# Kernel tuning notes

Measured on AMD Instinct MI355X. Metric: run time of the kernel, lower is better.

Reference implementation:

```python
import jax, jax.numpy as jnp
import numpy as np

J = 24          # SMPL_NR_JOINTS
H = 24          # hidden_dim
D_IN = 3        # input_dim (xyz)
SMPL_PARENTS = [-1, 0, 0, 0, 1, 2, 3, 4, 5, 6, 7, 8, 9, 9, 9, 12, 13, 14, 16, 17, 18, 19, 20, 21]

def _build_A():
    # undirected kinematic tree + self loops, row-normalized (mean aggregation)
    M = np.zeros((J, J), np.float32)
    for child, parent in enumerate(SMPL_PARENTS):
        if parent >= 0:
            M[child, parent] = 1.0
            M[parent, child] = 1.0
    M += np.eye(J, dtype=np.float32)
    M /= M.sum(axis=1, keepdims=True)
    return jnp.asarray(M)

A_NORM = _build_A()  # [J, J]

def setup_inputs() -> dict:
    key = jax.random.key(0)
    ks = jax.random.split(key, 12)
    B, S, T = 2048, 24, 24
    g = lambda k, shape, s=0.1: jax.random.normal(k, shape, dtype=jnp.float32) * s
    return {
        "src": g(ks[0], (B, S, J, D_IN), 1.0),
        "tgt": g(ks[1], (B, T, J, D_IN), 1.0),
        "We": g(ks[2], (H, D_IN)), "be": jnp.zeros((H,), jnp.float32),
        # gate order: 0=i, 1=f, 2=c, 3=o
        "Wxl": g(ks[3], (4, H, H)), "bxl": jnp.zeros((4, H), jnp.float32),
        "Wxr": g(ks[4], (4, H, H)),
        "Whl": g(ks[5], (4, H, H)), "bhl": jnp.zeros((4, H), jnp.float32),
        "Whr": g(ks[6], (4, H, H)),
        "wg": g(ks[7], (3, H)),   # peephole weights for i, f, o
        "bg": jnp.zeros((4, H), jnp.float32),
        "Wd": g(ks[8], (D_IN * J, H * J)), "bd": jnp.zeros((D_IN * J,), jnp.float32),
    }

def _gconv(x, Wl, bl, Wr):
    # x: [B, J, D]; mean-aggregate over fixed 24-node graph, then l(agg) + r(x)
    agg = jnp.einsum('ij,bjd->bid', A_NORM, x)
    return agg @ Wl.T + bl + x @ Wr.T

def _cell(X, h, c, Wxl, bxl, Wxr, Whl, bhl, Whr, wg, bg):
    gx = lambda g: _gconv(X, Wxl[g], bxl[g], Wxr[g])
    gh = lambda g: _gconv(h, Whl[g], bhl[g], Whr[g])
    i = jax.nn.sigmoid(gx(0) + gh(0) + wg[0] * c + bg[0])
    f = jax.nn.sigmoid(gx(1) + gh(1) + wg[1] * c + bg[1])
    c_new = f * c + i * jnp.tanh(gx(2) + gh(2) + bg[2])
    o = jax.nn.sigmoid(gx(3) + gh(3) + wg[2] * c_new + bg[3])
    h_new = o * jnp.tanh(c_new)
    return o, h_new, c_new

def reference(src, tgt, We, be, Wxl, bxl, Wxr, Whl, bhl, Whr, wg, bg, Wd, bd):
    B, S = src.shape[0], src.shape[1]
    T = tgt.shape[1]
    params = (Wxl, bxl, Wxr, Whl, bhl, Whr, wg, bg)
    enc = lambda x: jax.nn.relu(x @ We.T + be)  # [B, J, H]

    # --- warm-up over last 24 src frames (deterministic: encode only first step) ---
    X0 = enc(src[:, S - 24])
    h = jnp.zeros((B, J, H), src.dtype)
    c = jnp.zeros((B, J, H), src.dtype)
    out, h, c = _cell(X0, h, c, *params)

    def warm_step(carry, _):
        o_, h_, c_ = carry
        o_, h_, c_ = _cell(o_, h_, c_, *params)
        return (o_, h_, c_), None
    (out, h, c), _ = jax.lax.scan(warm_step, (out, h, c), None, length=23)

    # --- decode T steps: first input is enc(tgt[:,0]), then feed previous out ---
    out0, h, c = _cell(enc(tgt[:, 0]), h, c, *params)

    def dec_step(carry, _):
        o_, h_, c_ = carry
        o2, h2, c2 = _cell(o_, h_, c_, *params)
        return (o2, h2, c2), o2
    _, rest = jax.lax.scan(dec_step, (out0, h, c), None, length=T - 1)  # [T-1, B, J, H]

    seq = jnp.concatenate([out0[None], rest], axis=0)            # [T, B, J, H]
    outs = seq.transpose(1, 0, 2, 3).reshape(B, T, J * H)        # [B, T, 576]
    return outs @ Wd.T + bd                                      # [B, T, 72]
```

## Files before the change

### kernel.cpp

```cpp
#include <hip/hip_runtime.h>


typedef short  s16x8 __attribute__((ext_vector_type(8)));
typedef float  f32x4 __attribute__((ext_vector_type(4)));
typedef _Float16 f16x8 __attribute__((ext_vector_type(8)));

#define TPB 192
#define NB 2
#define PQ_OFF 0
#define UO_OFF 19968
#define SMEM_SZ 26880

#define BAR() do { asm volatile("s_waitcnt lgkmcnt(0)" ::: "memory"); \
                   __builtin_amdgcn_s_barrier(); } while (0)

__device__ __forceinline__ unsigned short f2h(float f) {
    _Float16 h = (_Float16)f;
    return *(unsigned short*)&h;
}
__device__ __forceinline__ unsigned int pkrtz(float a, float b) {
    auto h = __builtin_amdgcn_cvt_pkrtz(a, b);
    return *(unsigned int*)&h;
}
__device__ __forceinline__ float frcp(float x) { return __builtin_amdgcn_rcpf(x); }
__device__ __forceinline__ float sigm(float x) {
    float t = __expf(-x);
    return frcp(1.0f + t);
}
__device__ __forceinline__ float tanh_(float x) {
    float xc = fmaxf(x, -30.f);
    float t = __expf(-2.f * xc);
    return (1.f - t) * frcp(1.f + t);
}

extern "C" __global__ void __launch_bounds__(TPB, 3)
gclstm_main(const float* __restrict__ src,
            const float* __restrict__ tgt,
            const float* __restrict__ We,
            const float* __restrict__ be,
            const float* __restrict__ Wxl,
            const float* __restrict__ bxl,
            const float* __restrict__ Wxr,
            const float* __restrict__ Whl,
            const float* __restrict__ bhl,
            const float* __restrict__ Whr,
            const float* __restrict__ wg,
            const float* __restrict__ bg,
            unsigned short* __restrict__ seqh)
{
    __shared__ __align__(16) char smem[SMEM_SZ];
    unsigned short* PQt  = (unsigned short*)(smem + PQ_OFF);
    unsigned short* UO   = (unsigned short*)(smem + UO_OFF);
    unsigned int*   UO32 = (unsigned int*)(smem + UO_OFF);

    const int tid = threadIdx.x;
    const int b0 = blockIdx.x * NB;
    const int lane = tid & 63, wid = tid >> 6;
    const int l15 = lane & 15, quad = lane >> 4;

    const int par[24] = {-1,0,0,0,1,2,3,4,5,6,7,8,9,9,9,12,13,14,16,17,18,19,20,21};

    f16x8 w1f[4][2];
#pragma unroll
    for (int cj = 0; cj < 4; ++cj) {
        int np = (wid * 4 + cj) * 16 + l15;
        int path = np >= 96 ? 1 : 0;
        int nn = np - path * 96;
        int g = nn / 24, d = nn - g * 24;
        const float* Wx = path ? Wxr : Wxl;
        const float* Wh = path ? Whr : Whl;
#pragma unroll
        for (int kt = 0; kt < 2; ++kt) {
            f16x8 f;
#pragma unroll
            for (int kk = 0; kk < 8; ++kk) {
                int k = kt * 32 + quad * 8 + kk;
                float v = 0.f;
                if (k < 48) {
                    int df = k >> 1;
                    v = (k & 1) ? Wh[g * 576 + d * 24 + df] : Wx[g * 576 + d * 24 + df];
                }
                f[kk] = (_Float16)v;
            }
            w1f[cj][kt] = f;
        }
    }

    f16x8 mf[3];
    {
        int i = wid * 16 + l15;
        int si = i / 24, ji = i - si * 24;
        int cnt = 1 + (par[ji] >= 0 ? 1 : 0);
#pragma unroll
        for (int ch = 0; ch < 24; ++ch) cnt += (par[ch] == ji) ? 1 : 0;
        float cntf = (float)cnt;
#pragma unroll
        for (int kt = 0; kt < 3; ++kt) {
            f16x8 f;
#pragma unroll
            for (int kk = 0; kk < 8; ++kk) {
                int jp = kt * 32 + quad * 8 + kk;
                int sj = jp / 48;
                int rem = jp - sj * 48;
                int pz = rem / 24;
                int j = rem - pz * 24;
                float v = 0.f;
                if (sj == si) {
                    if (pz == 0) v = (j == ji || par[j] == ji || par[ji] == j) ? 1.f : 0.f;
                    else         v = (j == ji) ? cntf : 0.f;
                }
                f[kk] = (_Float16)v;
            }
            mf[kt] = f;
        }
    }

    const int d1 = l15;
    const int d2 = 16 + (l15 & 7);
    const bool lo = l15 < 8;
    float bC1[4], bC2[4], wv1[3], wv2[3];
#pragma unroll
    for (int g = 0; g < 4; ++g) {
        bC1[g] = bxl[g * 24 + d1] + bhl[g * 24 + d1] + bg[g * 24 + d1];
        bC2[g] = bxl[g * 24 + d2] + bhl[g * 24 + d2] + bg[g * 24 + d2];
    }
#pragma unroll
    for (int p = 0; p < 3; ++p) { wv1[p] = wg[p * 24 + d1]; wv2[p] = wg[p * 24 + d2]; }

    int rowR[4];
    float iwR[4];
    unsigned int sb[4];
#pragma unroll
    for (int rr = 0; rr < 4; ++rr) {
        int row = wid * 16 + quad * 4 + rr;
        rowR[rr] = row;
        int j = row % 24;
        int cnt = 1 + (par[j] >= 0 ? 1 : 0);
#pragma unroll
        for (int ch = 0; ch < 24; ++ch) cnt += (par[ch] == j) ? 1 : 0;
        iwR[rr] = cnt == 2 ? 0.5f : cnt == 3 ? (1.f / 3.f) : cnt == 4 ? 0.25f : 0.2f;
        sb[rr] = (unsigned int)((b0 + row / 24) * 13824 + j * 24);
    }
    int row2v[2]; float iw2v[2]; unsigned int sb2v[2];
#pragma unroll
    for (int e = 0; e < 2; ++e) {
        int rsel = lo ? e : e + 2;
        row2v[e] = rowR[rsel]; iw2v[e] = iwR[rsel]; sb2v[e] = sb[rsel];
    }

    float c1[4] = {0.f, 0.f, 0.f, 0.f};
    float c2[2] = {0.f, 0.f};

#pragma unroll
    for (int t = 0; t < 3; ++t) {
        int task = tid + t * TPB;
        int row = task / 12, dp = task - row * 12;
        int b = b0 + row / 24, j = row % 24;
        const float* sp = src + (size_t)b * 1728 + j * 3;
        float s0 = sp[0], s1 = sp[1], s2 = sp[2];
        int d = 2 * dp;
        float x0 = be[d] + s0 * We[d * 3] + s1 * We[d * 3 + 1] + s2 * We[d * 3 + 2];
        float x1 = be[d + 1] + s0 * We[d * 3 + 3] + s1 * We[d * 3 + 4] + s2 * We[d * 3 + 5];
        x0 = fmaxf(x0, 0.f); x1 = fmaxf(x1, 0.f);
        uint2 wv; wv.x = pkrtz(x0, 0.f); wv.y = pkrtz(x1, 0.f);
        *(uint2*)(UO32 + row * 36 + 2 * dp) = wv;
    }
    {
        int row = tid >> 2, c = tid & 3;
        uint2 z; z.x = 0u; z.y = 0u;
        *(uint2*)(UO32 + row * 36 + 24 + 2 * c) = z;
    }
    __syncthreads();

    for (int s = 0; s < 48; ++s) {
        if (s == 24) {
#pragma unroll
            for (int t = 0; t < 3; ++t) {
                int task = tid + t * TPB;
                int row = task / 12, dp = task - row * 12;
                int b = b0 + row / 24, j = row % 24;
                const float* tp = tgt + (size_t)b * 1728 + j * 3;
                float s0 = tp[0], s1 = tp[1], s2 = tp[2];
                int d = 2 * dp;
                float x0 = be[d] + s0 * We[d * 3] + s1 * We[d * 3 + 1] + s2 * We[d * 3 + 2];
                float x1 = be[d + 1] + s0 * We[d * 3 + 3] + s1 * We[d * 3 + 4]
                         + s2 * We[d * 3 + 5];
                x0 = fmaxf(x0, 0.f); x1 = fmaxf(x1, 0.f);
                UO[row * 72 + 4 * dp] = f2h(x0);
                UO[row * 72 + 4 * dp + 2] = f2h(x1);
            }
            BAR();
        }

        f32x4 acc1[3][4];
#pragma unroll
        for (int rt = 0; rt < 3; ++rt)
#pragma unroll
            for (int cj = 0; cj < 4; ++cj) acc1[rt][cj] = (f32x4)0.f;
#pragma unroll
        for (int kt = 0; kt < 2; ++kt) {
            f16x8 a[3];
#pragma unroll
            for (int rt = 0; rt < 3; ++rt)
                a[rt] = *(const f16x8*)(UO + (rt * 16 + l15) * 72 + kt * 32 + quad * 8);
#pragma unroll
            for (int rt = 0; rt < 3; ++rt)
#pragma unroll
                for (int cj = 0; cj < 4; ++cj)
                    acc1[rt][cj] = __builtin_amdgcn_mfma_f32_16x16x32_f16(a[rt], w1f[cj][kt], acc1[rt][cj], 0, 0, 0);
        }
#pragma unroll
        for (int rt = 0; rt < 3; ++rt)
#pragma unroll
            for (int cj = 0; cj < 4; ++cj) {
                int np = (wid * 4 + cj) * 16 + l15;
                int path = np >= 96;
                int nn = np - (path ? 96 : 0);
                int jg = rt * 16 + quad * 4;
                int col = (path ? 24 : 0) + jg + (jg >= 24 ? 24 : 0);
                uint2 wv;
                wv.x = pkrtz(acc1[rt][cj][0], acc1[rt][cj][1]);
                wv.y = pkrtz(acc1[rt][cj][2], acc1[rt][cj][3]);
                *(uint2*)(PQt + nn * 104 + col) = wv;
            }
        BAR();

        f32x4 acc2[6];
#pragma unroll
        for (int nt = 0; nt < 6; ++nt) acc2[nt] = (f32x4)0.f;
#pragma unroll
        for (int kt = 0; kt < 3; ++kt) {
            if (kt == 2 && wid == 0) continue;
            if (kt == 0 && wid == 2) continue;
            f16x8 bf[6];
#pragma unroll
            for (int nt = 0; nt < 6; ++nt)
                bf[nt] = *(const f16x8*)(PQt + (nt * 16 + l15) * 104 + kt * 32 + quad * 8);
#pragma unroll
            for (int nt = 0; nt < 6; ++nt)
                acc2[nt] = __builtin_amdgcn_mfma_f32_16x16x32_f16(mf[kt], bf[nt], acc2[nt], 0, 0, 0);
        }

        const int so = (s - 24) * 576;

#pragma unroll
        for (int rr = 0; rr < 4; ++rr) {
            float pf_s = __shfl_xor(lo ? acc2[2][rr] : acc2[1][rr], 8);
            float po_s = __shfl_xor(lo ? acc2[5][rr] : acc2[4][rr], 8);
            float iw = iwR[rr];
            int row = rowR[rr];
            float c = c1[rr];
            float pi = fmaf(iw, acc2[0][rr], bC1[0]);
            float pf = fmaf(iw, pf_s, bC1[1]);
            float pc = fmaf(iw, acc2[3][rr], bC1[2]);
            float po = fmaf(iw, po_s, bC1[3]);
            float iv = sigm(fmaf(wv1[0], c, pi));
            float fv = sigm(fmaf(wv1[1], c, pf));
            float cn = fmaf(fv, c, iv * tanh_(pc));
            float ov = sigm(fmaf(wv1[2], cn, po));
            c1[rr] = cn;
            float hv = ov * tanh_(cn);
            unsigned int pk = pkrtz(ov, hv);
            UO32[row * 36 + d1] = pk;
            if (s >= 24) seqh[sb[rr] + (unsigned int)(so + d1)] = (unsigned short)pk;
        }
#pragma unroll
        for (int e = 0; e < 2; ++e) {
            float sA = __shfl_xor(lo ? acc2[1][e + 2] : acc2[2][e], 8);
            float sB = __shfl_xor(lo ? acc2[4][e + 2] : acc2[5][e], 8);
            float g0 = lo ? acc2[1][e] : sA;
            float g1 = lo ? sA : acc2[2][e + 2];
            float g2 = lo ? acc2[4][e] : sB;
            float g3 = lo ? sB : acc2[5][e + 2];
            float iw = iw2v[e];
            int row = row2v[e];
            float c = c2[e];
            float pi = fmaf(iw, g0, bC2[0]);
            float pf = fmaf(iw, g1, bC2[1]);
            float pc = fmaf(iw, g2, bC2[2]);
            float po = fmaf(iw, g3, bC2[3]);
            float iv = sigm(fmaf(wv2[0], c, pi));
            float fv = sigm(fmaf(wv2[1], c, pf));
            float cn = fmaf(fv, c, iv * tanh_(pc));
            float ov = sigm(fmaf(wv2[2], cn, po));
            c2[e] = cn;
            float hv = ov * tanh_(cn);
            unsigned int pk = pkrtz(ov, hv);
            UO32[row * 36 + d2] = pk;
            if (s >= 24) seqh[sb2v[e] + (unsigned int)(so + d2)] = (unsigned short)pk;
        }
        BAR();
    }
}

extern "C" __global__ void __launch_bounds__(256)
wd_conv(const float* __restrict__ Wd, unsigned short* __restrict__ WdH)
{
    int i = blockIdx.x * 256 + threadIdx.x;
    if (i < 46080) {
        int n = i / 576, k = i - n * 576;
        WdH[i] = (n < 72) ? f2h(Wd[n * 576 + k]) : (unsigned short)0;
    }
}

template <int PRECONV>
__global__ void __launch_bounds__(256, 6)
gclstm_proj(const unsigned short* __restrict__ seqh,
            const unsigned short* __restrict__ WdH,
            const float* __restrict__ Wd,
            const float* __restrict__ bd,
            float* __restrict__ out)
{
    __shared__ unsigned short SQ[32 * 104];
    __shared__ unsigned short WH[80 * 104];

    const int tid = threadIdx.x;
    const int R0 = blockIdx.x * 32;
    const int lane = tid & 63, wid = tid >> 6;
    const int l15 = lane & 15, quad = lane >> 4;
    const int rt = wid & 1;
    const int c0 = (wid < 2) ? 0 : 3;
    const int nct = (wid < 2) ? 3 : 2;

    f32x4 acc[3];
#pragma unroll
    for (int j = 0; j < 3; ++j) acc[j] = (f32x4)0.f;

    if (PRECONV) {
        s16x8 sreg[2], wreg[4];
        const int r0s = tid / 12, c0s = tid - r0s * 12;
        const int i1 = tid + 256;
        const int r1s = i1 / 12, c1s = i1 - r1s * 12;
        sreg[0] = *(const s16x8*)(seqh + (size_t)(R0 + r0s) * 576 + (size_t)(c0s * 8));
        if (tid < 128)
            sreg[1] = *(const s16x8*)(seqh + (size_t)(R0 + r1s) * 576 + (size_t)(c1s * 8));
#pragma unroll
        for (int j = 0; j < 4; ++j) {
            int i = tid + j * 256;
            if (i < 960) { int n = i / 12, c8 = i - n * 12;
                wreg[j] = *(const s16x8*)(WdH + (size_t)n * 576 + (size_t)(c8 * 8)); }
        }
        for (int kc = 0; kc < 576; kc += 96) {
            *(s16x8*)(&SQ[r0s * 104 + c0s * 8]) = sreg[0];
            if (tid < 128) *(s16x8*)(&SQ[r1s * 104 + c1s * 8]) = sreg[1];
#pragma unroll
            for (int j = 0; j < 4; ++j) {
                int i = tid + j * 256;
                if (i < 960) { int n = i / 12, c8 = i - n * 12;
                    *(s16x8*)(&WH[n * 104 + c8 * 8]) = wreg[j]; }
            }
            BAR();
            if (kc + 96 < 576) {
                sreg[0] = *(const s16x8*)(seqh + (size_t)(R0 + r0s) * 576 + (size_t)(kc + 96 + c0s * 8));
                if (tid < 128)
                    sreg[1] = *(const s16x8*)(seqh + (size_t)(R0 + r1s) * 576 + (size_t)(kc + 96 + c1s * 8));
#pragma unroll
                for (int j = 0; j < 4; ++j) {
                    int i = tid + j * 256;
                    if (i < 960) { int n = i / 12, c8 = i - n * 12;
                        wreg[j] = *(const s16x8*)(WdH + (size_t)n * 576 + (size_t)(kc + 96 + c8 * 8)); }
                }
            }
#pragma unroll
            for (int kt = 0; kt < 3; ++kt) {
                int koff = kt * 32 + quad * 8;
                f16x8 a = *(const f16x8*)(&SQ[(rt * 16 + l15) * 104 + koff]);
#pragma unroll
                for (int j = 0; j < 3; ++j) {
                    if (j < nct) {
                        f16x8 b = *(const f16x8*)(&WH[((c0 + j) * 16 + l15) * 104 + koff]);
                        acc[j] = __builtin_amdgcn_mfma_f32_16x16x32_f16(a, b, acc[j], 0, 0, 0);
                    }
                }
            }
            BAR();
        }
    } else {
        for (int kc = 0; kc < 576; kc += 96) {
            __syncthreads();
            for (int i = tid; i < 384; i += 256) {
                int r = i / 12, c8 = i - r * 12;
                *(s16x8*)(&SQ[r * 104 + c8 * 8]) =
                    *(const s16x8*)(seqh + (size_t)(R0 + r) * 576 + (size_t)(kc + c8 * 8));
            }
            for (int i = tid; i < 7680; i += 256) {
                int n = i / 96, kk = i - n * 96;
                float v = (n < 72) ? Wd[(size_t)n * 576 + (size_t)(kc + kk)] : 0.f;
                WH[n * 104 + kk] = f2h(v);
            }
            __syncthreads();
#pragma unroll
            for (int kt = 0; kt < 3; ++kt) {
                int koff = kt * 32 + quad * 8;
                f16x8 a = *(const f16x8*)(&SQ[(rt * 16 + l15) * 104 + koff]);
#pragma unroll
                for (int j = 0; j < 3; ++j) {
                    if (j < nct) {
                        f16x8 b = *(const f16x8*)(&WH[((c0 + j) * 16 + l15) * 104 + koff]);
                        acc[j] = __builtin_amdgcn_mfma_f32_16x16x32_f16(a, b, acc[j], 0, 0, 0);
                    }
                }
            }
        }
    }

#pragma unroll
    for (int j = 0; j < 3; ++j) {
        if (j < nct) {
            int n = (c0 + j) * 16 + l15;
            if (n < 72) {
                float bv = bd[n];
                int rbase = R0 + rt * 16 + quad * 4;
#pragma unroll
                for (int r = 0; r < 4; ++r)
                    out[(size_t)(rbase + r) * 72 + (size_t)n] = acc[j][r] + bv;
            }
        }
    }
}

extern "C" void kernel_launch(void* const* d_in, const int* in_sizes, int n_in,
                              void* d_out, int out_size, void* d_ws, size_t ws_size,
                              hipStream_t stream)
{
    const float* src = (const float*)d_in[0];
    const float* tgt = (const float*)d_in[1];
    const float* We  = (const float*)d_in[2];
    const float* be  = (const float*)d_in[3];
    const float* Wxl = (const float*)d_in[4];
    const float* bxl = (const float*)d_in[5];
    const float* Wxr = (const float*)d_in[6];
    const float* Whl = (const float*)d_in[7];
    const float* bhl = (const float*)d_in[8];
    const float* Whr = (const float*)d_in[9];
    const float* wg  = (const float*)d_in[10];
    const float* bg  = (const float*)d_in[11];
    const float* Wd  = (const float*)d_in[12];
    const float* bd  = (const float*)d_in[13];
    float* out = (float*)d_out;
    unsigned short* seqh = (unsigned short*)d_ws;

    const size_t seq_bytes = (size_t)2048 * 24 * 576 * 2;
    unsigned short* WdH = (unsigned short*)((char*)d_ws + seq_bytes);
    const bool preconv = ws_size >= seq_bytes + (size_t)80 * 576 * 2;

    if (preconv)
        wd_conv<<<dim3(180), dim3(256), 0, stream>>>(Wd, WdH);
    gclstm_main<<<dim3(1024), dim3(TPB), 0, stream>>>(
        src, tgt, We, be, Wxl, bxl, Wxr, Whl, bhl, Whr, wg, bg, seqh);
    if (preconv)
        gclstm_proj<1><<<dim3(1536), dim3(256), 0, stream>>>(seqh, WdH, Wd, bd, out);
    else
        gclstm_proj<0><<<dim3(1536), dim3(256), 0, stream>>>(seqh, nullptr, Wd, bd, out);
}
```

Measured before the change: 328.3 us.

## Replace LDS-staged projection GEMM with register-direct MFMA loads

New measurement: 352.2 us. 7.3% more time.

```diff
diff --git a/kernel.cpp b/kernel.cpp
--- a/kernel.cpp
+++ b/kernel.cpp
@@ -303,13 +303,58 @@
     }
 }
 
-template <int PRECONV>
+__global__ void __launch_bounds__(256, 4)
+gclstm_proj_reg(const unsigned short* __restrict__ seqh,
+                const unsigned short* __restrict__ WdH,
+                const float* __restrict__ bd,
+                float* __restrict__ out)
+{
+    const int tid = threadIdx.x;
+    const int R0 = blockIdx.x * 64;
+    const int lane = tid & 63, wid = tid >> 6;
+    const int l15 = lane & 15, quad = lane >> 4;
+
+    const unsigned short* arow = seqh + (size_t)(R0 + wid * 16 + l15) * 576;
+    f32x4 acc[5];
+#pragma unroll
+    for (int j = 0; j < 5; ++j) acc[j] = (f32x4)0.f;
+
+#pragma unroll
+    for (int kc = 0; kc < 576; kc += 96) {
+        f16x8 a[3], b[5][3];
+#pragma unroll
+        for (int kt = 0; kt < 3; ++kt) {
+            int koff = kc + kt * 32 + quad * 8;
+            a[kt] = *(const f16x8*)(arow + koff);
+#pragma unroll
+            for (int j = 0; j < 5; ++j)
+                b[j][kt] = *(const f16x8*)(WdH + (size_t)(j * 16 + l15) * 576 + koff);
+        }
+#pragma unroll
+        for (int kt = 0; kt < 3; ++kt)
+#pragma unroll
+            for (int j = 0; j < 5; ++j)
+                acc[j] = __builtin_amdgcn_mfma_f32_16x16x32_f16(a[kt], b[j][kt], acc[j], 0, 0, 0);
+    }
+
+#pragma unroll
+    for (int j = 0; j < 5; ++j) {
+        int n = j * 16 + l15;
+        if (n < 72) {
+            float bv = bd[n];
+            int rbase = R0 + wid * 16 + quad * 4;
+#pragma unroll
+            for (int r = 0; r < 4; ++r)
+                out[(size_t)(rbase + r) * 72 + (size_t)n] = acc[j][r] + bv;
+        }
+    }
+}
+
 __global__ void __launch_bounds__(256, 6)
-gclstm_proj(const unsigned short* __restrict__ seqh,
-            const unsigned short* __restrict__ WdH,
-            const float* __restrict__ Wd,
-            const float* __restrict__ bd,
-            float* __restrict__ out)
+gclstm_proj_lds(const unsigned short* __restrict__ seqh,
+                const float* __restrict__ Wd,
+                const float* __restrict__ bd,
+                float* __restrict__ out)
 {
     __shared__ unsigned short SQ[32 * 104];
     __shared__ unsigned short WH[80 * 104];
@@ -326,79 +371,28 @@
 #pragma unroll
     for (int j = 0; j < 3; ++j) acc[j] = (f32x4)0.f;
 
-    if (PRECONV) {
-        s16x8 sreg[2], wreg[4];
-        const int r0s = tid / 12, c0s = tid - r0s * 12;
-        const int i1 = tid + 256;
-        const int r1s = i1 / 12, c1s = i1 - r1s * 12;
-        sreg[0] = *(const s16x8*)(seqh + (size_t)(R0 + r0s) * 576 + (size_t)(c0s * 8));
-        if (tid < 128)
-            sreg[1] = *(const s16x8*)(seqh + (size_t)(R0 + r1s) * 576 + (size_t)(c1s * 8));
-#pragma unroll
-        for (int j = 0; j < 4; ++j) {
-            int i = tid + j * 256;
-            if (i < 960) { int n = i / 12, c8 = i - n * 12;
-                wreg[j] = *(const s16x8*)(WdH + (size_t)n * 576 + (size_t)(c8 * 8)); }
-        }
-        for (int kc = 0; kc < 576; kc += 96) {
-            *(s16x8*)(&SQ[r0s * 104 + c0s * 8]) = sreg[0];
-            if (tid < 128) *(s16x8*)(&SQ[r1s * 104 + c1s * 8]) = sreg[1];
-#pragma unroll
-            for (int j = 0; j < 4; ++j) {
-                int i = tid + j * 256;
-                if (i < 960) { int n = i / 12, c8 = i - n * 12;
-                    *(s16x8*)(&WH[n * 104 + c8 * 8]) = wreg[j]; }
-            }
-            BAR();
-            if (kc + 96 < 576) {
-                sreg[0] = *(const s16x8*)(seqh + (size_t)(R0 + r0s) * 576 + (size_t)(kc + 96 + c0s * 8));
-                if (tid < 128)
-                    sreg[1] = *(const s16x8*)(seqh + (size_t)(R0 + r1s) * 576 + (size_t)(kc + 96 + c1s * 8));
-#pragma unroll
-                for (int j = 0; j < 4; ++j) {
-                    int i = tid + j * 256;
-                    if (i < 960) { int n = i / 12, c8 = i - n * 12;
-                        wreg[j] = *(const s16x8*)(WdH + (size_t)n * 576 + (size_t)(kc + 96 + c8 * 8)); }
-                }
-            }
-#pragma unroll
-            for (int kt = 0; kt < 3; ++kt) {
-                int koff = kt * 32 + quad * 8;
-                f16x8 a = *(const f16x8*)(&SQ[(rt * 16 + l15) * 104 + koff]);
-#pragma unroll
-                for (int j = 0; j < 3; ++j) {
-                    if (j < nct) {
-                        f16x8 b = *(const f16x8*)(&WH[((c0 + j) * 16 + l15) * 104 + koff]);
-                        acc[j] = __builtin_amdgcn_mfma_f32_16x16x32_f16(a, b, acc[j], 0, 0, 0);
-                    }
-                }
-            }
-            BAR();
-        }
-    } else {
-        for (int kc = 0; kc < 576; kc += 96) {
-            __syncthreads();
-            for (int i = tid; i < 384; i += 256) {
-                int r = i / 12, c8 = i - r * 12;
-                *(s16x8*)(&SQ[r * 104 + c8 * 8]) =
-                    *(const s16x8*)(seqh + (size_t)(R0 + r) * 576 + (size_t)(kc + c8 * 8));
-            }
-            for (int i = tid; i < 7680; i += 256) {
-                int n = i / 96, kk = i - n * 96;
-                float v = (n < 72) ? Wd[(size_t)n * 576 + (size_t)(kc + kk)] : 0.f;
-                WH[n * 104 + kk] = f2h(v);
-            }
-            __syncthreads();
-#pragma unroll
-            for (int kt = 0; kt < 3; ++kt) {
-                int koff = kt * 32 + quad * 8;
-                f16x8 a = *(const f16x8*)(&SQ[(rt * 16 + l15) * 104 + koff]);
-#pragma unroll
-                for (int j = 0; j < 3; ++j) {
-                    if (j < nct) {
-                        f16x8 b = *(const f16x8*)(&WH[((c0 + j) * 16 + l15) * 104 + koff]);
-                        acc[j] = __builtin_amdgcn_mfma_f32_16x16x32_f16(a, b, acc[j], 0, 0, 0);
-                    }
+    for (int kc = 0; kc < 576; kc += 96) {
+        __syncthreads();
+        for (int i = tid; i < 384; i += 256) {
+            int r = i / 12, c8 = i - r * 12;
+            *(s16x8*)(&SQ[r * 104 + c8 * 8]) =
+                *(const s16x8*)(seqh + (size_t)(R0 + r) * 576 + (size_t)(kc + c8 * 8));
+        }
+        for (int i = tid; i < 7680; i += 256) {
+            int n = i / 96, kk = i - n * 96;
+            float v = (n < 72) ? Wd[(size_t)n * 576 + (size_t)(kc + kk)] : 0.f;
+            WH[n * 104 + kk] = f2h(v);
+        }
+        __syncthreads();
+#pragma unroll
+        for (int kt = 0; kt < 3; ++kt) {
+            int koff = kt * 32 + quad * 8;
+            f16x8 a = *(const f16x8*)(&SQ[(rt * 16 + l15) * 104 + koff]);
+#pragma unroll
+            for (int j = 0; j < 3; ++j) {
+                if (j < nct) {
+                    f16x8 b = *(const f16x8*)(&WH[((c0 + j) * 16 + l15) * 104 + koff]);
+                    acc[j] = __builtin_amdgcn_mfma_f32_16x16x32_f16(a, b, acc[j], 0, 0, 0);
                 }
             }
         }
@@ -449,7 +443,7 @@
     gclstm_main<<<dim3(1024), dim3(TPB), 0, stream>>>(
         src, tgt, We, be, Wxl, bxl, Wxr, Whl, bhl, Whr, wg, bg, seqh);
     if (preconv)
-        gclstm_proj<1><<<dim3(1536), dim3(256), 0, stream>>>(seqh, WdH, Wd, bd, out);
+        gclstm_proj_reg<<<dim3(768), dim3(256), 0, stream>>>(seqh, WdH, bd, out);
     else
-        gclstm_proj<0><<<dim3(1536), dim3(256), 0, stream>>>(seqh, nullptr, Wd, bd, out);
-}
+        gclstm_proj_lds<<<dim3(1536), dim3(256), 0, stream>>>(seqh, Wd, bd, out);
+}
```
